# Performance work log

Measured on AMD Instinct MI355X. Metric: run time of the kernel, lower is better.

## Reference

```python
import jax, jax.numpy as jnp
import numpy as np


def _bilinear_align_corners(g, H, W):
    # g: [B, 1, h, w] -> [B, 1, H, W], matching F.interpolate(mode='bilinear', align_corners=True)
    B, C, h, w = g.shape
    ys = jnp.linspace(0.0, h - 1.0, H)
    xs = jnp.linspace(0.0, w - 1.0, W)
    y0 = jnp.clip(jnp.floor(ys).astype(jnp.int32), 0, h - 1)
    y1 = jnp.clip(y0 + 1, 0, h - 1)
    x0 = jnp.clip(jnp.floor(xs).astype(jnp.int32), 0, w - 1)
    x1 = jnp.clip(x0 + 1, 0, w - 1)
    wy = (ys - y0.astype(g.dtype))[:, None]          # [H,1]
    wx = (xs - x0.astype(g.dtype))[None, :]          # [1,W]
    g00 = g[:, :, y0][:, :, :, x0]                   # [B,C,H,W]
    g01 = g[:, :, y0][:, :, :, x1]
    g10 = g[:, :, y1][:, :, :, x0]
    g11 = g[:, :, y1][:, :, :, x1]
    top = g00 * (1 - wx) + g01 * wx
    bot = g10 * (1 - wx) + g11 * wx
    return top * (1 - wy) + bot * wy


def setup_inputs() -> dict:
    key = jax.random.key(0)
    ks = jax.random.split(key, 6)
    B, C, H, W = 4, 256, 64, 64
    Cq = C // 8
    return {
        "x": jax.random.normal(ks[0], (B, C, H, W), jnp.float32),
        "guiding_map0": jax.random.normal(ks[1], (B, 1, 32, 32), jnp.float32),
        "Wq": jax.random.normal(ks[2], (Cq, C), jnp.float32) * 0.05,
        "bq": jnp.zeros((Cq,), jnp.float32),
        "Wk": jax.random.normal(ks[3], (Cq, C), jnp.float32) * 0.05,
        "bk": jnp.zeros((Cq,), jnp.float32),
        "Wv": jax.random.normal(ks[4], (C, C), jnp.float32) * 0.05,
        "bv": jnp.zeros((C,), jnp.float32),
        "gamma": jnp.ones((1,), jnp.float32),
    }


def reference(x, guiding_map0, Wq, bq, Wk, bk, Wv, bv, gamma):
    B, C, H, W = x.shape
    N = H * W
    gm = jax.nn.sigmoid(_bilinear_align_corners(guiding_map0, H, W))  # [B,1,H,W]
    gate = 1.0 + gm
    # 1x1 convs as channel contractions, then multiplicative gating
    q = (jnp.einsum('oc,bchw->bohw', Wq, x) + bq[None, :, None, None]) * gate
    k = (jnp.einsum('oc,bchw->bohw', Wk, x) + bk[None, :, None, None]) * gate
    v = (jnp.einsum('oc,bchw->bohw', Wv, x) + bv[None, :, None, None]) * gate
    q = q.reshape(B, -1, N)   # [B,Cq,N]
    k = k.reshape(B, -1, N)   # [B,Cq,N]
    v = v.reshape(B, C, N)    # [B,C,N]
    energy = jnp.einsum('bcm,bcn->bmn', q, k)        # [B,N,N]
    attention = jax.nn.softmax(energy, axis=-1)
    # out[b,c,m] = sum_n v[b,c,n] * attn[b,m,n]
    out = jnp.einsum('bcn,bmn->bcm', v, attention).reshape(B, C, H, W)
    return gamma[0] * out + x
```

## Files before the change

### kernel.cpp

```cpp
#include <hip/hip_runtime.h>
#include <math.h>

#define NN 4096
#define CC 256

typedef unsigned short u16;
typedef float f32x16 __attribute__((ext_vector_type(16)));
typedef short s16x8 __attribute__((ext_vector_type(8)));

#define ZERO16 {0.f,0.f,0.f,0.f,0.f,0.f,0.f,0.f,0.f,0.f,0.f,0.f,0.f,0.f,0.f,0.f}

#define GLOAD_LDS16(gsrc, ldst) \
    __builtin_amdgcn_global_load_lds((const __attribute__((address_space(1))) unsigned int*)(gsrc), \
                                     (__attribute__((address_space(3))) unsigned int*)(ldst), 16, 0, 0)

__device__ __forceinline__ u16 f2bf(float f){
    unsigned u = __float_as_uint(f);
    return (u16)((u + 0x7fffu + ((u >> 16) & 1u)) >> 16);
}
__device__ __forceinline__ float bf2f(u16 h){
    return __uint_as_float(((unsigned)h) << 16);
}

__global__ __launch_bounds__(256) void gate_kernel(
    const float* __restrict__ g0, const float* __restrict__ Wq,
    const float* __restrict__ Wk, const float* __restrict__ Wv,
    float* __restrict__ gate,
    u16* __restrict__ wqhi, u16* __restrict__ wqlo,
    u16* __restrict__ wkhi, u16* __restrict__ wklo,
    u16* __restrict__ wvbf)
{
    int idx = blockIdx.x * 256 + threadIdx.x;
    int b  = idx >> 12;
    int hw = idx & 4095;
    int h = hw >> 6, w = hw & 63;
    float ys = h * (31.0f / 63.0f);
    float xs = w * (31.0f / 63.0f);
    int y0 = (int)ys, x0 = (int)xs;
    int y1 = min(y0 + 1, 31), x1 = min(x0 + 1, 31);
    float wy = ys - (float)y0, wx = xs - (float)x0;
    const float* g = g0 + b * 1024;
    float g00 = g[y0 * 32 + x0], g01 = g[y0 * 32 + x1];
    float g10 = g[y1 * 32 + x0], g11 = g[y1 * 32 + x1];
    float top = g00 * (1.0f - wx) + g01 * wx;
    float bot = g10 * (1.0f - wx) + g11 * wx;
    float val = top * (1.0f - wy) + bot * wy;
    gate[idx] = 1.0f + 1.0f / (1.0f + __expf(-val));

    if (idx < 8192) {
        float a = Wq[idx];
        u16 ha = f2bf(a);
        wqhi[idx] = ha; wqlo[idx] = f2bf(a - bf2f(ha));
        float c = Wk[idx];
        u16 hc = f2bf(c);
        wkhi[idx] = hc; wklo[idx] = f2bf(c - bf2f(hc));
    }
#pragma unroll
    for (int j = 0; j < 4; j++)
        wvbf[idx + j * 16384] = f2bf(Wv[idx + j * 16384]);
}

__global__ __launch_bounds__(512, 4) void qkv_kernel(
    const float* __restrict__ x,
    const u16* __restrict__ wqhi, const u16* __restrict__ wqlo,
    const u16* __restrict__ wkhi, const u16* __restrict__ wklo,
    const u16* __restrict__ wvbf,
    const float* __restrict__ bq, const float* __restrict__ bk,
    const float* __restrict__ bv, const float* __restrict__ gate,
    u16* __restrict__ qhi, u16* __restrict__ qlo,
    u16* __restrict__ khi, u16* __restrict__ klo,
    u16* __restrict__ vbf)
{
    __shared__ u16 Xh[64 * 256];
    __shared__ u16 Xl[64 * 256];
    int bid = blockIdx.x;
    int b  = (bid >> 1) & 3;
    int nt = (bid >> 3) | ((bid & 1) << 5);
    int n0 = nt * 64;
    int tid = threadIdx.x;

    {
        const float* xb = x + (size_t)b * CC * NN;
        int cb = tid >> 4;
        int nc = tid & 15;
#pragma unroll
        for (int j = 0; j < 8; j++) {
            int c = cb + 32 * j;
            float4 xv = *(const float4*)(xb + (size_t)c * NN + n0 + nc * 4);
            float xf[4] = {xv.x, xv.y, xv.z, xv.w};
#pragma unroll
            for (int i = 0; i < 4; i++) {
                int n = nc * 4 + i;
                u16 hv = f2bf(xf[i]);
                u16 lv = f2bf(xf[i] - bf2f(hv));
                int u = n * 256 + (c ^ ((n & 31) << 3));
                Xh[u] = hv; Xl[u] = lv;
            }
        }
    }
    __syncthreads();

    int w = tid >> 6, l = tid & 63;
    int l5 = l >> 5, l31 = l & 31;

    if (w < 4) {
        int proj = w & 1, nh = w >> 1;
        const u16* Whi = proj ? wkhi : wqhi;
        const u16* Wlo = proj ? wklo : wqlo;
        const float* bias = proj ? bk : bq;
        u16* dhi = proj ? khi : qhi;
        u16* dlo = proj ? klo : qlo;
        int nl = nh * 32 + l31;
        int swz = (nl & 31) << 3;

        f32x16 acc = ZERO16;
        for (int ks = 0; ks < 16; ks++) {
            int c0 = ks * 16 + 8 * l5;
            s16x8 whi = *(const s16x8*)(Whi + l31 * 256 + c0);
            s16x8 wlo = *(const s16x8*)(Wlo + l31 * 256 + c0);
            int u = nl * 256 + (c0 ^ swz);
            s16x8 xh = *(const s16x8*)(Xh + u);
            s16x8 xl = *(const s16x8*)(Xl + u);
            acc = __builtin_amdgcn_mfma_f32_32x32x16_bf16(whi, xh, acc, 0, 0, 0);
            acc = __builtin_amdgcn_mfma_f32_32x32x16_bf16(whi, xl, acc, 0, 0, 0);
            acc = __builtin_amdgcn_mfma_f32_32x32x16_bf16(wlo, xh, acc, 0, 0, 0);
        }
        int n = n0 + nl;
        float g = gate[b * NN + n];
        size_t rowo = ((size_t)b * NN + n) * 32;
#pragma unroll
        for (int t = 0; t < 4; t++) {
            int ob = 8 * t + 4 * l5;
            unsigned h01 = 0, h23 = 0, l01 = 0, l23 = 0;
#pragma unroll
            for (int j = 0; j < 4; j++) {
                float v = (acc[4 * t + j] + bias[ob + j]) * g;
                u16 h = f2bf(v);
                u16 lo = f2bf(v - bf2f(h));
                if (j < 2) { h01 |= ((unsigned)h) << (16 * j); l01 |= ((unsigned)lo) << (16 * j); }
                else       { h23 |= ((unsigned)h) << (16 * (j - 2)); l23 |= ((unsigned)lo) << (16 * (j - 2)); }
            }
            *(unsigned*)(dhi + rowo + ob)     = h01;
            *(unsigned*)(dhi + rowo + ob + 2) = h23;
            *(unsigned*)(dlo + rowo + ob)     = l01;
            *(unsigned*)(dlo + rowo + ob + 2) = l23;
        }
    } else {
        int vw = w - 4;
        int cB = vw * 64;
        int swz = (l31 & 31) << 3;
        f32x16 acc[2][2] = {{ZERO16, ZERO16}, {ZERO16, ZERO16}};
        for (int ks = 0; ks < 16; ks++) {
            int c0 = ks * 16 + 8 * l5;
            int u0 = l31 * 256 + (c0 ^ swz);
            s16x8 xh0 = *(const s16x8*)(Xh + u0);
            s16x8 xh1 = *(const s16x8*)(Xh + u0 + 32 * 256);
#pragma unroll
            for (int ct = 0; ct < 2; ct++) {
                s16x8 wv = *(const s16x8*)(wvbf + (size_t)(cB + ct * 32 + l31) * 256 + c0);
                acc[ct][0] = __builtin_amdgcn_mfma_f32_32x32x16_bf16(wv, xh0, acc[ct][0], 0, 0, 0);
                acc[ct][1] = __builtin_amdgcn_mfma_f32_32x32x16_bf16(wv, xh1, acc[ct][1], 0, 0, 0);
            }
        }
#pragma unroll
        for (int nh2 = 0; nh2 < 2; nh2++) {
            int n = n0 + nh2 * 32 + l31;
            float g = gate[b * NN + n];
#pragma unroll
            for (int ct = 0; ct < 2; ct++) {
#pragma unroll
                for (int r = 0; r < 16; r++) {
                    int c = cB + ct * 32 + (r & 3) + 8 * (r >> 2) + 4 * l5;
                    vbf[((size_t)b * CC + c) * NN + n] = f2bf((acc[ct][nh2][r] + bv[c]) * g);
                }
            }
        }
    }
}

__global__ __launch_bounds__(512, 4) void stats_kernel(
    const u16* __restrict__ qhi, const u16* __restrict__ qlo,
    const u16* __restrict__ khi, const u16* __restrict__ klo,
    float* __restrict__ lse)
{
    __shared__ float Sm[8][2][16], Ss[8][2][16];
    int bid = blockIdx.x;
    int b  = (bid >> 1) & 3;
    int mt = (bid >> 3) | ((bid & 1) << 5);
    int tid = threadIdx.x;
    int w = tid >> 6, l = tid & 63;
    int l5 = l >> 5, l31 = l & 31;
    int strip = w & 1, ns = w >> 1;
    int mS = mt * 64 + strip * 32;

    size_t qo = ((size_t)b * NN + mS + l31) * 32 + 8 * l5;
    s16x8 qh0 = *(const s16x8*)(qhi + qo), ql0 = *(const s16x8*)(qlo + qo);
    s16x8 qh1 = *(const s16x8*)(qhi + qo + 16), ql1 = *(const s16x8*)(qlo + qo + 16);

    float rmax[16], rsum[16];
#pragma unroll
    for (int r = 0; r < 16; r++) { rmax[r] = -1e30f; rsum[r] = 0.f; }

    for (int it = 0; it < 32; it++) {
        size_t ko = ((size_t)b * NN + it * 128 + ns * 32 + l31) * 32 + 8 * l5;
        s16x8 kh0 = *(const s16x8*)(khi + ko), kl0 = *(const s16x8*)(klo + ko);
        s16x8 kh1 = *(const s16x8*)(khi + ko + 16), kl1 = *(const s16x8*)(klo + ko + 16);
        f32x16 a = ZERO16;
        a = __builtin_amdgcn_mfma_f32_32x32x16_bf16(ql0, kh0, a, 0, 0, 0);
        a = __builtin_amdgcn_mfma_f32_32x32x16_bf16(qh0, kl0, a, 0, 0, 0);
        a = __builtin_amdgcn_mfma_f32_32x32x16_bf16(qh0, kh0, a, 0, 0, 0);
        a = __builtin_amdgcn_mfma_f32_32x32x16_bf16(ql1, kh1, a, 0, 0, 0);
        a = __builtin_amdgcn_mfma_f32_32x32x16_bf16(qh1, kl1, a, 0, 0, 0);
        a = __builtin_amdgcn_mfma_f32_32x32x16_bf16(qh1, kh1, a, 0, 0, 0);
#pragma unroll
        for (int r = 0; r < 16; r++) {
            float nm = fmaxf(rmax[r], a[r]);
            rsum[r] = rsum[r] * __expf(rmax[r] - nm) + __expf(a[r] - nm);
            rmax[r] = nm;
        }
    }

#pragma unroll
    for (int r = 0; r < 16; r++) {
#pragma unroll
        for (int off = 16; off >= 1; off >>= 1) {
            float om = __shfl_xor(rmax[r], off);
            float os = __shfl_xor(rsum[r], off);
            float nm = fmaxf(rmax[r], om);
            rsum[r] = rsum[r] * __expf(rmax[r] - nm) + os * __expf(om - nm);
            rmax[r] = nm;
        }
    }
    if (l31 == 0) {
#pragma unroll
        for (int r = 0; r < 16; r++) { Sm[w][l5][r] = rmax[r]; Ss[w][l5][r] = rsum[r]; }
    }
    __syncthreads();
    if (w < 2 && l31 == 0) {
#pragma unroll
        for (int r = 0; r < 16; r++) {
            float M = -1e30f;
#pragma unroll
            for (int j = 0; j < 4; j++) M = fmaxf(M, Sm[w + 2 * j][l5][r]);
            float S = 0.f;
#pragma unroll
            for (int j = 0; j < 4; j++)
                S += Ss[w + 2 * j][l5][r] * __expf(Sm[w + 2 * j][l5][r] - M);
            int m = mt * 64 + w * 32 + (r & 3) + 8 * (r >> 2) + 4 * l5;
            lse[b * NN + m] = M + __logf(S);
        }
    }
}

__global__ __launch_bounds__(512, 2) void out_kernel(
    const u16* __restrict__ qhi, const u16* __restrict__ qlo,
    const u16* __restrict__ khi, const u16* __restrict__ klo,
    const u16* __restrict__ vbf, const float* __restrict__ lse,
    const float* __restrict__ x, const float* __restrict__ gamma,
    float* __restrict__ out)
{
    __shared__ u16 Vl[256 * 128];
    __shared__ u16 Pl[64 * 128];
    int bid = blockIdx.x;
    int b  = (bid >> 1) & 3;
    int mt = (bid >> 3) | ((bid & 1) << 5);
    int tid = threadIdx.x;
    int w = tid >> 6, l = tid & 63;
    int l5 = l >> 5, l31 = l & 31;
    int strip = w & 1, cq = w >> 1;
    int mS = mt * 64 + strip * 32;

    size_t qo = ((size_t)b * NN + mS + l31) * 32 + 8 * l5;
    s16x8 qh0 = *(const s16x8*)(qhi + qo), ql0 = *(const s16x8*)(qlo + qo);
    s16x8 qh1 = *(const s16x8*)(qhi + qo + 16), ql1 = *(const s16x8*)(qlo + qo + 16);

    float lr[16];
#pragma unroll
    for (int r = 0; r < 16; r++)
        lr[r] = lse[b * NN + mS + (r & 3) + 8 * (r >> 2) + 4 * l5];

    f32x16 acc[2] = {ZERO16, ZERO16};
    const u16* vb = vbf + (size_t)b * CC * NN;

    for (int it = 0; it < 32; it++) {
        int n0 = it * 128;
#pragma unroll
        for (int j = 0; j < 8; j++) {
            int s = w * 512 + j * 64 + l;
            int c = s >> 4, chk = s & 15;
            const u16* src = vb + (size_t)c * NN + n0 + ((chk * 8) ^ ((c & 15) << 3));
            GLOAD_LDS16(src, Vl + (size_t)(w * 512 + j * 64) * 8);
        }
        {
            size_t ko = ((size_t)b * NN + n0 + cq * 32 + l31) * 32 + 8 * l5;
            s16x8 kh0 = *(const s16x8*)(khi + ko), kl0 = *(const s16x8*)(klo + ko);
            s16x8 kh1 = *(const s16x8*)(khi + ko + 16), kl1 = *(const s16x8*)(klo + ko + 16);
            f32x16 a = ZERO16;
            a = __builtin_amdgcn_mfma_f32_32x32x16_bf16(ql0, kh0, a, 0, 0, 0);
            a = __builtin_amdgcn_mfma_f32_32x32x16_bf16(qh0, kl0, a, 0, 0, 0);
            a = __builtin_amdgcn_mfma_f32_32x32x16_bf16(qh0, kh0, a, 0, 0, 0);
            a = __builtin_amdgcn_mfma_f32_32x32x16_bf16(ql1, kh1, a, 0, 0, 0);
            a = __builtin_amdgcn_mfma_f32_32x32x16_bf16(qh1, kl1, a, 0, 0, 0);
            a = __builtin_amdgcn_mfma_f32_32x32x16_bf16(qh1, kh1, a, 0, 0, 0);
#pragma unroll
            for (int r = 0; r < 16; r++) {
                float p = __expf(a[r] - lr[r]);
                int m = strip * 32 + (r & 3) + 8 * (r >> 2) + 4 * l5;
                int nc = cq * 32 + l31;
                Pl[m * 128 + (nc ^ ((m & 15) << 3))] = f2bf(p);
            }
        }
        __syncthreads();
#pragma unroll
        for (int ks = 0; ks < 8; ks++) {
            int col = ks * 16 + 8 * l5;
            int mr = strip * 32 + l31;
            s16x8 pa = *(const s16x8*)(Pl + mr * 128 + (col ^ ((mr & 15) << 3)));
            int c0r = cq * 64 + l31, c1r = cq * 64 + 32 + l31;
            s16x8 vv0 = *(const s16x8*)(Vl + c0r * 128 + (col ^ ((c0r & 15) << 3)));
            s16x8 vv1 = *(const s16x8*)(Vl + c1r * 128 + (col ^ ((c1r & 15) << 3)));
            acc[0] = __builtin_amdgcn_mfma_f32_32x32x16_bf16(pa, vv0, acc[0], 0, 0, 0);
            acc[1] = __builtin_amdgcn_mfma_f32_32x32x16_bf16(pa, vv1, acc[1], 0, 0, 0);
        }
        __syncthreads();
    }

    float gm = gamma[0];
#pragma unroll
    for (int cs = 0; cs < 2; cs++) {
        int c = cq * 64 + cs * 32 + l31;
#pragma unroll
        for (int t = 0; t < 4; t++) {
            size_t o = ((size_t)b * CC + c) * NN + mS + 8 * t + 4 * l5;
            float4 x4 = *(const float4*)(x + o);
            float4 r4;
            r4.x = fmaf(gm, acc[cs][4 * t + 0], x4.x);
            r4.y = fmaf(gm, acc[cs][4 * t + 1], x4.y);
            r4.z = fmaf(gm, acc[cs][4 * t + 2], x4.z);
            r4.w = fmaf(gm, acc[cs][4 * t + 3], x4.w);
            *(float4*)(out + o) = r4;
        }
    }
}

extern "C" void kernel_launch(void* const* d_in, const int* in_sizes, int n_in,
                              void* d_out, int out_size, void* d_ws, size_t ws_size,
                              hipStream_t stream)
{
    const float* x     = (const float*)d_in[0];
    const float* g0    = (const float*)d_in[1];
    const float* Wq    = (const float*)d_in[2];
    const float* bq    = (const float*)d_in[3];
    const float* Wk    = (const float*)d_in[4];
    const float* bk    = (const float*)d_in[5];
    const float* Wv    = (const float*)d_in[6];
    const float* bv    = (const float*)d_in[7];
    const float* gamma = (const float*)d_in[8];
    float* out = (float*)d_out;

    char* p = (char*)d_ws;
    u16* qhi = (u16*)p; p += (size_t)4 * NN * 32 * 2;
    u16* qlo = (u16*)p; p += (size_t)4 * NN * 32 * 2;
    u16* khi = (u16*)p; p += (size_t)4 * NN * 32 * 2;
    u16* klo = (u16*)p; p += (size_t)4 * NN * 32 * 2;
    u16* vbf = (u16*)p; p += (size_t)4 * CC * NN * 2;
    float* gate = (float*)p; p += (size_t)4 * NN * 4;
    float* lse  = (float*)p; p += (size_t)4 * NN * 4;
    u16* wqhi = (u16*)p; p += 8192 * 2;
    u16* wqlo = (u16*)p; p += 8192 * 2;
    u16* wkhi = (u16*)p; p += 8192 * 2;
    u16* wklo = (u16*)p; p += 8192 * 2;
    u16* wvbf = (u16*)p; p += 65536 * 2;

    hipLaunchKernelGGL(gate_kernel, dim3(64), dim3(256), 0, stream,
                       g0, Wq, Wk, Wv, gate, wqhi, wqlo, wkhi, wklo, wvbf);
    hipLaunchKernelGGL(qkv_kernel, dim3(256), dim3(512), 0, stream,
                       x, wqhi, wqlo, wkhi, wklo, wvbf, bq, bk, bv, gate,
                       qhi, qlo, khi, klo, vbf);
    hipLaunchKernelGGL(stats_kernel, dim3(256), dim3(512), 0, stream,
                       qhi, qlo, khi, klo, lse);
    hipLaunchKernelGGL(out_kernel, dim3(256), dim3(512), 0, stream,
                       qhi, qlo, khi, klo, vbf, lse, x, gamma, out);
}
```

Baseline: 137.1 us.

## Split attention output kernel across channel halves and pack Q/K hi-lo rows

The output kernel now splits the 256 value channels into two halves per block. This doubles the grid to 512 blocks, halves the V tile in shared memory, and raises the launch-bounds occupancy target. Q and K hi/lo bf16 parts are stored interleaved in a single 64-element row, so each row's loads come from one contiguous region. The trade-off is that each block recomputes the QK^T scores and exponentials for its half, so that part of the work is duplicated.

```diff
diff --git a/kernel.cpp b/kernel.cpp
--- a/kernel.cpp
+++ b/kernel.cpp
@@ -67,8 +67,7 @@
     const u16* __restrict__ wvbf,
     const float* __restrict__ bq, const float* __restrict__ bk,
     const float* __restrict__ bv, const float* __restrict__ gate,
-    u16* __restrict__ qhi, u16* __restrict__ qlo,
-    u16* __restrict__ khi, u16* __restrict__ klo,
+    u16* __restrict__ qpk, u16* __restrict__ kpk,
     u16* __restrict__ vbf)
 {
     __shared__ u16 Xh[64 * 256];
@@ -108,8 +107,7 @@
         const u16* Whi = proj ? wkhi : wqhi;
         const u16* Wlo = proj ? wklo : wqlo;
         const float* bias = proj ? bk : bq;
-        u16* dhi = proj ? khi : qhi;
-        u16* dlo = proj ? klo : qlo;
+        u16* dpk = proj ? kpk : qpk;
         int nl = nh * 32 + l31;
         int swz = (nl & 31) << 3;
 
@@ -127,7 +125,7 @@
         }
         int n = n0 + nl;
         float g = gate[b * NN + n];
-        size_t rowo = ((size_t)b * NN + n) * 32;
+        size_t rowo = ((size_t)b * NN + n) * 64;
 #pragma unroll
         for (int t = 0; t < 4; t++) {
             int ob = 8 * t + 4 * l5;
@@ -140,10 +138,10 @@
                 if (j < 2) { h01 |= ((unsigned)h) << (16 * j); l01 |= ((unsigned)lo) << (16 * j); }
                 else       { h23 |= ((unsigned)h) << (16 * (j - 2)); l23 |= ((unsigned)lo) << (16 * (j - 2)); }
             }
-            *(unsigned*)(dhi + rowo + ob)     = h01;
-            *(unsigned*)(dhi + rowo + ob + 2) = h23;
-            *(unsigned*)(dlo + rowo + ob)     = l01;
-            *(unsigned*)(dlo + rowo + ob + 2) = l23;
+            *(unsigned*)(dpk + rowo + ob)          = h01;
+            *(unsigned*)(dpk + rowo + ob + 2)      = h23;
+            *(unsigned*)(dpk + rowo + 32 + ob)     = l01;
+            *(unsigned*)(dpk + rowo + 32 + ob + 2) = l23;
         }
     } else {
         int vw = w - 4;
@@ -179,8 +177,7 @@
 }
 
 __global__ __launch_bounds__(512, 4) void stats_kernel(
-    const u16* __restrict__ qhi, const u16* __restrict__ qlo,
-    const u16* __restrict__ khi, const u16* __restrict__ klo,
+    const u16* __restrict__ qpk, const u16* __restrict__ kpk,
     float* __restrict__ lse)
 {
     __shared__ float Sm[8][2][16], Ss[8][2][16];
@@ -193,18 +190,18 @@
     int strip = w & 1, ns = w >> 1;
     int mS = mt * 64 + strip * 32;
 
-    size_t qo = ((size_t)b * NN + mS + l31) * 32 + 8 * l5;
-    s16x8 qh0 = *(const s16x8*)(qhi + qo), ql0 = *(const s16x8*)(qlo + qo);
-    s16x8 qh1 = *(const s16x8*)(qhi + qo + 16), ql1 = *(const s16x8*)(qlo + qo + 16);
+    size_t qo = ((size_t)b * NN + mS + l31) * 64 + 8 * l5;
+    s16x8 qh0 = *(const s16x8*)(qpk + qo),      ql0 = *(const s16x8*)(qpk + qo + 32);
+    s16x8 qh1 = *(const s16x8*)(qpk + qo + 16), ql1 = *(const s16x8*)(qpk + qo + 48);
 
     float rmax[16], rsum[16];
 #pragma unroll
     for (int r = 0; r < 16; r++) { rmax[r] = -1e30f; rsum[r] = 0.f; }
 
     for (int it = 0; it < 32; it++) {
-        size_t ko = ((size_t)b * NN + it * 128 + ns * 32 + l31) * 32 + 8 * l5;
-        s16x8 kh0 = *(const s16x8*)(khi + ko), kl0 = *(const s16x8*)(klo + ko);
-        s16x8 kh1 = *(const s16x8*)(khi + ko + 16), kl1 = *(const s16x8*)(klo + ko + 16);
+        size_t ko = ((size_t)b * NN + it * 128 + ns * 32 + l31) * 64 + 8 * l5;
+        s16x8 kh0 = *(const s16x8*)(kpk + ko),      kl0 = *(const s16x8*)(kpk + ko + 32);
+        s16x8 kh1 = *(const s16x8*)(kpk + ko + 16), kl1 = *(const s16x8*)(kpk + ko + 48);
         f32x16 a = ZERO16;
         a = __builtin_amdgcn_mfma_f32_32x32x16_bf16(ql0, kh0, a, 0, 0, 0);
         a = __builtin_amdgcn_mfma_f32_32x32x16_bf16(qh0, kl0, a, 0, 0, 0);
@@ -252,49 +249,50 @@
     }
 }
 
-__global__ __launch_bounds__(512, 2) void out_kernel(
-    const u16* __restrict__ qhi, const u16* __restrict__ qlo,
-    const u16* __restrict__ khi, const u16* __restrict__ klo,
+__global__ __launch_bounds__(512, 6) void out_kernel(
+    const u16* __restrict__ qpk, const u16* __restrict__ kpk,
     const u16* __restrict__ vbf, const float* __restrict__ lse,
     const float* __restrict__ x, const float* __restrict__ gamma,
     float* __restrict__ out)
 {
-    __shared__ u16 Vl[256 * 128];
+    __shared__ u16 Vl[128 * 128];
     __shared__ u16 Pl[64 * 128];
     int bid = blockIdx.x;
-    int b  = (bid >> 1) & 3;
-    int mt = (bid >> 3) | ((bid & 1) << 5);
+    int sub = bid & 7;
+    int b  = sub >> 1;
+    int ch = sub & 1;
+    int mt = bid >> 3;
     int tid = threadIdx.x;
     int w = tid >> 6, l = tid & 63;
     int l5 = l >> 5, l31 = l & 31;
     int strip = w & 1, cq = w >> 1;
     int mS = mt * 64 + strip * 32;
 
-    size_t qo = ((size_t)b * NN + mS + l31) * 32 + 8 * l5;
-    s16x8 qh0 = *(const s16x8*)(qhi + qo), ql0 = *(const s16x8*)(qlo + qo);
-    s16x8 qh1 = *(const s16x8*)(qhi + qo + 16), ql1 = *(const s16x8*)(qlo + qo + 16);
+    size_t qo = ((size_t)b * NN + mS + l31) * 64 + 8 * l5;
+    s16x8 qh0 = *(const s16x8*)(qpk + qo),      ql0 = *(const s16x8*)(qpk + qo + 32);
+    s16x8 qh1 = *(const s16x8*)(qpk + qo + 16), ql1 = *(const s16x8*)(qpk + qo + 48);
 
     float lr[16];
 #pragma unroll
     for (int r = 0; r < 16; r++)
         lr[r] = lse[b * NN + mS + (r & 3) + 8 * (r >> 2) + 4 * l5];
 
-    f32x16 acc[2] = {ZERO16, ZERO16};
-    const u16* vb = vbf + (size_t)b * CC * NN;
+    f32x16 acc = ZERO16;
+    const u16* vb = vbf + ((size_t)b * CC + ch * 128) * NN;
 
     for (int it = 0; it < 32; it++) {
         int n0 = it * 128;
 #pragma unroll
-        for (int j = 0; j < 8; j++) {
-            int s = w * 512 + j * 64 + l;
+        for (int j = 0; j < 4; j++) {
+            int s = j * 512 + w * 64 + l;
             int c = s >> 4, chk = s & 15;
             const u16* src = vb + (size_t)c * NN + n0 + ((chk * 8) ^ ((c & 15) << 3));
-            GLOAD_LDS16(src, Vl + (size_t)(w * 512 + j * 64) * 8);
+            GLOAD_LDS16(src, Vl + (size_t)(j * 512 + w * 64) * 8);
         }
         {
-            size_t ko = ((size_t)b * NN + n0 + cq * 32 + l31) * 32 + 8 * l5;
-            s16x8 kh0 = *(const s16x8*)(khi + ko), kl0 = *(const s16x8*)(klo + ko);
-            s16x8 kh1 = *(const s16x8*)(khi + ko + 16), kl1 = *(const s16x8*)(klo + ko + 16);
+            size_t ko = ((size_t)b * NN + n0 + cq * 32 + l31) * 64 + 8 * l5;
+            s16x8 kh0 = *(const s16x8*)(kpk + ko),      kl0 = *(const s16x8*)(kpk + ko + 32);
+            s16x8 kh1 = *(const s16x8*)(kpk + ko + 16), kl1 = *(const s16x8*)(kpk + ko + 48);
             f32x16 a = ZERO16;
             a = __builtin_amdgcn_mfma_f32_32x32x16_bf16(ql0, kh0, a, 0, 0, 0);
             a = __builtin_amdgcn_mfma_f32_32x32x16_bf16(qh0, kl0, a, 0, 0, 0);
@@ -315,31 +313,26 @@
         for (int ks = 0; ks < 8; ks++) {
             int col = ks * 16 + 8 * l5;
             int mr = strip * 32 + l31;
+            int cr = cq * 32 + l31;
             s16x8 pa = *(const s16x8*)(Pl + mr * 128 + (col ^ ((mr & 15) << 3)));
-            int c0r = cq * 64 + l31, c1r = cq * 64 + 32 + l31;
-            s16x8 vv0 = *(const s16x8*)(Vl + c0r * 128 + (col ^ ((c0r & 15) << 3)));
-            s16x8 vv1 = *(const s16x8*)(Vl + c1r * 128 + (col ^ ((c1r & 15) << 3)));
-            acc[0] = __builtin_amdgcn_mfma_f32_32x32x16_bf16(pa, vv0, acc[0], 0, 0, 0);
-            acc[1] = __builtin_amdgcn_mfma_f32_32x32x16_bf16(pa, vv1, acc[1], 0, 0, 0);
+            s16x8 vv = *(const s16x8*)(Vl + cr * 128 + (col ^ ((cr & 15) << 3)));
+            acc = __builtin_amdgcn_mfma_f32_32x32x16_bf16(pa, vv, acc, 0, 0, 0);
         }
         __syncthreads();
     }
 
     float gm = gamma[0];
-#pragma unroll
-    for (int cs = 0; cs < 2; cs++) {
-        int c = cq * 64 + cs * 32 + l31;
-#pragma unroll
-        for (int t = 0; t < 4; t++) {
-            size_t o = ((size_t)b * CC + c) * NN + mS + 8 * t + 4 * l5;
-            float4 x4 = *(const float4*)(x + o);
-            float4 r4;
-            r4.x = fmaf(gm, acc[cs][4 * t + 0], x4.x);
-            r4.y = fmaf(gm, acc[cs][4 * t + 1], x4.y);
-            r4.z = fmaf(gm, acc[cs][4 * t + 2], x4.z);
-            r4.w = fmaf(gm, acc[cs][4 * t + 3], x4.w);
-            *(float4*)(out + o) = r4;
-        }
+    int c = ch * 128 + cq * 32 + l31;
+#pragma unroll
+    for (int t = 0; t < 4; t++) {
+        size_t o = ((size_t)b * CC + c) * NN + mS + 8 * t + 4 * l5;
+        float4 x4 = *(const float4*)(x + o);
+        float4 r4;
+        r4.x = fmaf(gm, acc[4 * t + 0], x4.x);
+        r4.y = fmaf(gm, acc[4 * t + 1], x4.y);
+        r4.z = fmaf(gm, acc[4 * t + 2], x4.z);
+        r4.w = fmaf(gm, acc[4 * t + 3], x4.w);
+        *(float4*)(out + o) = r4;
     }
 }
 
@@ -359,10 +352,8 @@
     float* out = (float*)d_out;
 
     char* p = (char*)d_ws;
-    u16* qhi = (u16*)p; p += (size_t)4 * NN * 32 * 2;
-    u16* qlo = (u16*)p; p += (size_t)4 * NN * 32 * 2;
-    u16* khi = (u16*)p; p += (size_t)4 * NN * 32 * 2;
-    u16* klo = (u16*)p; p += (size_t)4 * NN * 32 * 2;
+    u16* qpk = (u16*)p; p += (size_t)4 * NN * 64 * 2;
+    u16* kpk = (u16*)p; p += (size_t)4 * NN * 64 * 2;
     u16* vbf = (u16*)p; p += (size_t)4 * CC * NN * 2;
     float* gate = (float*)p; p += (size_t)4 * NN * 4;
     float* lse  = (float*)p; p += (size_t)4 * NN * 4;
@@ -376,9 +367,9 @@
                        g0, Wq, Wk, Wv, gate, wqhi, wqlo, wkhi, wklo, wvbf);
     hipLaunchKernelGGL(qkv_kernel, dim3(256), dim3(512), 0, stream,
                        x, wqhi, wqlo, wkhi, wklo, wvbf, bq, bk, bv, gate,
-                       qhi, qlo, khi, klo, vbf);
+                       qpk, kpk, vbf);
     hipLaunchKernelGGL(stats_kernel, dim3(256), dim3(512), 0, stream,
-                       qhi, qlo, khi, klo, lse);
-    hipLaunchKernelGGL(out_kernel, dim3(256), dim3(512), 0, stream,
-                       qhi, qlo, khi, klo, vbf, lse, x, gamma, out);
-}
+                       qpk, kpk, lse);
+    hipLaunchKernelGGL(out_kernel, dim3(512), dim3(512), 0, stream,
+                       qpk, kpk, vbf, lse, x, gamma, out);
+}
```

Measured after the change: 360.4 us. 163% more time.
